# Kernel optimization log

Measured on AMD Instinct MI355X. Metric: run time of the kernel, lower is better.

Reference implementation:

```python
import jax, jax.numpy as jnp
import numpy as np

# Model dims: batch, num_patches, patch_dim, emb_dim, heads, layers, ffn, vocab, grid
B, N, PD, D, H, L, F, V, G = 4, 1024, 768, 768, 12, 6, 3072, 1024, 32
HD = D // H  # head dim = 64


def setup_inputs() -> dict:
    key = jax.random.key(0)
    ks = jax.random.split(key, 22)
    s = 0.02
    r = lambda k, shp: jax.random.normal(k, shp, dtype=jnp.float32) * s
    return {
        "patches": jax.random.normal(ks[0], (B, N, PD), dtype=jnp.float32),
        "mask": jax.random.bernoulli(ks[1], 0.3, (B, N)),
        "mask_token": r(ks[2], (PD,)),
        "patch_w": r(ks[3], (D, PD)),
        "patch_b": jnp.zeros((D,), jnp.float32),
        "pos_emb": r(ks[4], (N, D)),
        "rel_bias": r(ks[5], (2 * G - 1, 2 * G - 1)),
        # stacked per-layer params [L, ...]
        "in_w": r(ks[6], (L, 3 * D, D)),
        "in_b": jnp.zeros((L, 3 * D), jnp.float32),
        "attn_ow": r(ks[7], (L, D, D)),
        "attn_ob": jnp.zeros((L, D), jnp.float32),
        "ln1_s": jnp.ones((L, D), jnp.float32),
        "ln1_b": jnp.zeros((L, D), jnp.float32),
        "ffn_w1": r(ks[8], (L, F, D)),
        "ffn_b1": jnp.zeros((L, F), jnp.float32),
        "ffn_w2": r(ks[9], (L, D, F)),
        "ffn_b2": jnp.zeros((L, D), jnp.float32),
        "ln2_s": jnp.ones((L, D), jnp.float32),
        "ln2_b": jnp.zeros((L, D), jnp.float32),
        "head_w": r(ks[10], (V, D)),
        "head_b": jnp.zeros((V,), jnp.float32),
    }


def _layer_norm(x, scale, bias, eps=1e-5):
    mu = jnp.mean(x, axis=-1, keepdims=True)
    var = jnp.mean(jnp.square(x - mu), axis=-1, keepdims=True)
    return (x - mu) * jax.lax.rsqrt(var + eps) * scale + bias


def _rel_bias(rel_bias):
    # gathered Swin-style relative position bias -> [N, N]
    idx = jnp.arange(N)
    rows, cols = idx // G, idx % G
    ir = rows[:, None] - rows[None, :] + (G - 1)
    ic = cols[:, None] - cols[None, :] + (G - 1)
    return rel_bias[ir, ic]


def reference(patches, mask, mask_token, patch_w, patch_b, pos_emb, rel_bias,
              in_w, in_b, attn_ow, attn_ob, ln1_s, ln1_b,
              ffn_w1, ffn_b1, ffn_w2, ffn_b2, ln2_s, ln2_b, head_w, head_b):
    # replace masked patches with mask_token, project, add abs pos emb
    x = jnp.where(mask[:, :, None], mask_token, patches)
    x = x @ patch_w.T + patch_b + pos_emb  # [B,N,D]
    bias = _rel_bias(rel_bias)  # [N,N] additive attention bias
    scale = 1.0 / np.sqrt(HD).astype(np.float32)
    for l in range(L):
        qkv = x @ in_w[l].T + in_b[l]  # [B,N,3D]
        q, k, v = jnp.split(qkv, 3, axis=-1)
        split_heads = lambda t: t.reshape(B, N, H, HD).transpose(0, 2, 1, 3)
        q, k, v = split_heads(q), split_heads(k), split_heads(v)
        scores = jnp.einsum('bhqd,bhkd->bhqk', q, k) * scale + bias
        attn = jax.nn.softmax(scores, axis=-1)
        o = jnp.einsum('bhqk,bhkd->bhqd', attn, v)
        o = o.transpose(0, 2, 1, 3).reshape(B, N, D) @ attn_ow[l].T + attn_ob[l]
        x = _layer_norm(x + o, ln1_s[l], ln1_b[l])
        h = jax.nn.gelu(x @ ffn_w1[l].T + ffn_b1[l], approximate=False)
        x = _layer_norm(x + h @ ffn_w2[l].T + ffn_b2[l], ln2_s[l], ln2_b[l])
    logits = x @ head_w.T + head_b  # [B,N,V] (dropout = identity in eval)
    return logits, mask
```

## Files before the change

### kernel.cpp

```cpp
#include <hip/hip_runtime.h>
#include <hip/hip_bf16.h>
#include <stdint.h>


#define BM 64
#define BN 64
#define BK 32

using u16 = unsigned short;
typedef __attribute__((ext_vector_type(8))) short short8;
typedef __attribute__((ext_vector_type(4))) float f32x4;
typedef __attribute__((ext_vector_type(4))) u16 u16x4;

#define GPTR(p) ((const __attribute__((address_space(1))) void*)(p))
#define LPTR(p) ((__attribute__((address_space(3))) void*)(p))

__device__ __forceinline__ float b2f(u16 u){
  union { unsigned int i; float f; } x; x.i = ((unsigned int)u) << 16; return x.f;
}
__device__ __forceinline__ u16 f2b(float f){
  f = fminf(fmaxf(f, -448.0f), 448.0f);
  union { float f; unsigned int i; } x; x.f = f;
  unsigned int r = x.i + 0x7FFFu + ((x.i >> 16) & 1u);
  return (u16)(r >> 16);
}

__global__ __launch_bounds__(256) void detect_k(const u16* __restrict__ mk, int* __restrict__ mode){
  __shared__ int f[3];
  int tid = threadIdx.x;
  if (tid < 3) f[tid] = 0;
  __syncthreads();
  for (int i = tid; i < 2048; i += 256){
    u16 u = mk[i];
    if (u == 256 || u == 257) atomicOr(&f[0], 1);
    if (u == 0x3F80){ if ((i & 1) == 0) atomicOr(&f[1], 1); else atomicOr(&f[2], 1); }
  }
  __syncthreads();
  if (tid == 0){
    int m;
    if (f[0]) m = 0;
    else if (f[1]) m = 1;
    else if (f[2]) m = 2;
    else m = 3;
    *mode = m;
  }
}

__device__ __forceinline__ bool mask_at(const void* mk, int mode, int i){
  if (mode == 0) return ((const unsigned char*)mk)[i] != 0;
  if (mode == 1) return ((const u16*)mk)[i] != 0;
  if (mode == 2) return ((const float*)mk)[i] != 0.0f;
  return ((const int*)mk)[i] != 0;
}

__global__ __launch_bounds__(256) void wconv_k(const float* __restrict__ src, u16* __restrict__ dst){
  long i = ((long)blockIdx.x * 256 + threadIdx.x) * 4;
  float4 v = *(const float4*)(src + i);
  u16x4 o; o.x = f2b(v.x); o.y = f2b(v.y); o.z = f2b(v.z); o.w = f2b(v.w);
  *(u16x4*)(dst + i) = o;
}

__global__ __launch_bounds__(256) void embed_k(const float* __restrict__ patches, const void* __restrict__ mask,
                                               const int* __restrict__ mode, const float* __restrict__ mtok,
                                               u16* __restrict__ MP){
  int row = blockIdx.x;
  bool m = mask_at(mask, *mode, row);
  int tid = threadIdx.x;
  long base = (long)row * 768;
  #pragma unroll
  for (int i = 0; i < 3; i++){
    int p = tid + i * 256;
    MP[base + p] = f2b(m ? mtok[p] : patches[base + p]);
  }
}

__global__ __launch_bounds__(256) void maskout_k(const void* __restrict__ mask, const int* __restrict__ mode,
                                                 float* __restrict__ out){
  int i = blockIdx.x * 256 + threadIdx.x;
  out[i] = mask_at(mask, *mode, i) ? 1.0f : 0.0f;
}

__global__ __launch_bounds__(256) void ln_k(const u16* __restrict__ XR, u16* __restrict__ X,
                                            const float* __restrict__ s, const float* __restrict__ b){
  int row = blockIdx.x;
  int tid = threadIdx.x;
  const u16* xr = XR + (long)row * 768;
  float v0 = b2f(xr[tid]), v1 = b2f(xr[tid + 256]), v2 = b2f(xr[tid + 512]);
  float sum = v0 + v1 + v2, sq = v0 * v0 + v1 * v1 + v2 * v2;
  #pragma unroll
  for (int off = 32; off; off >>= 1){ sum += __shfl_xor(sum, off); sq += __shfl_xor(sq, off); }
  __shared__ float ls[4], lq[4];
  int wave = tid >> 6, lane = tid & 63;
  if (lane == 0){ ls[wave] = sum; lq[wave] = sq; }
  __syncthreads();
  sum = ls[0] + ls[1] + ls[2] + ls[3];
  sq  = lq[0] + lq[1] + lq[2] + lq[3];
  float mu = sum * (1.0f / 768.0f);
  float var = fmaxf(sq * (1.0f / 768.0f) - mu * mu, 0.0f);
  float rs = rsqrtf(var + 1e-5f);
  u16* xo = X + (long)row * 768;
  xo[tid]       = f2b((v0 - mu) * rs * s[tid]       + b[tid]);
  xo[tid + 256] = f2b((v1 - mu) * rs * s[tid + 256] + b[tid + 256]);
  xo[tid + 512] = f2b((v2 - mu) * rs * s[tid + 512] + b[tid + 512]);
}

__global__ __launch_bounds__(256) void softmax_k(u16* __restrict__ S){
  long row = (long)blockIdx.x * 4 + (threadIdx.x >> 6);
  u16* p = S + row * 1024;
  int lane = threadIdx.x & 63;
  short8 a = *(const short8*)&p[lane * 16];
  short8 b = *(const short8*)&p[lane * 16 + 8];
  float v[16]; float mx = -1e30f;
  #pragma unroll
  for (int i = 0; i < 8; i++){ v[i] = b2f((u16)a[i]); v[i + 8] = b2f((u16)b[i]); }
  #pragma unroll
  for (int i = 0; i < 16; i++) mx = fmaxf(mx, v[i]);
  #pragma unroll
  for (int off = 32; off; off >>= 1) mx = fmaxf(mx, __shfl_xor(mx, off));
  float sum = 0.0f;
  #pragma unroll
  for (int i = 0; i < 16; i++){ v[i] = __expf(v[i] - mx); sum += v[i]; }
  #pragma unroll
  for (int off = 32; off; off >>= 1) sum += __shfl_xor(sum, off);
  float inv = 1.0f / sum;
  #pragma unroll
  for (int i = 0; i < 8; i++){ a[i] = (short)f2b(v[i] * inv); b[i] = (short)f2b(v[i + 8] * inv); }
  *(short8*)&p[lane * 16] = a;
  *(short8*)&p[lane * 16 + 8] = b;
}

struct GP {
  const u16* A; const u16* W; u16* C; float* Cf;
  const float* bias; const float* relb; const float* pose;
  const u16* resid;
  u16* Cv;
  long sAz, sWz, sCz;
  int lda, ldw, ldc;
  int N, K;
  int wclamp, zBase;
  float scale;
};

template<int EPI>
__global__ __launch_bounds__(256)
void gemm_k(GP g){
  __shared__ __align__(16) u16 As[3][BM * BK];
  __shared__ __align__(16) u16 Bs[3][BN * BK];
  const int tid  = threadIdx.x;
  const int wave = tid >> 6, lane = tid & 63;
  const int quad = lane >> 4, l16 = lane & 15;
  const int wm = wave >> 1, wn = wave & 1;

  const int gx = gridDim.x;
  const int nwg = gx * gridDim.y;
  int bid = blockIdx.y * gx + blockIdx.x;
  {
    const int q = nwg >> 3, r = nwg & 7;
    const int xcd = bid & 7, loc = bid >> 3;
    bid = (xcd < r ? xcd * (q + 1) : r * (q + 1) + (xcd - r) * q) + loc;
  }
  const int m0 = (bid / gx) * BM;
  const int n0 = (bid % gx) * BN;
  const int z = blockIdx.z;

  const u16* Ab;
  const u16* Wb;
  if constexpr (EPI == 1){
    int hh = g.zBase + z;
    int b = hh / 12, h = hh - b * 12;
    Ab = g.A + (long)b * 1572864 + h * 64;
    Wb = Ab + 768;
  } else {
    Ab = g.A + (long)z * g.sAz;
    Wb = g.W + (long)z * g.sWz;
  }

  f32x4 acc[2][2];
  #pragma unroll
  for (int i = 0; i < 2; i++)
    #pragma unroll
    for (int j = 0; j < 2; j++) acc[i][j] = (f32x4){0.f, 0.f, 0.f, 0.f};

  const int c0 = wave * 64 + lane;
  const int arow = c0 >> 2, aslot = (c0 & 3) ^ (arow & 3);
  const u16* a0 = Ab + (long)(m0 + arow) * g.lda + aslot * 8;
  const u16* w0 = Wb + (long)min(n0 + arow, g.wclamp) * g.ldw + aslot * 8;
  const int o0 = wave * 512;

  const int nt = g.K / BK;

  #define STAGE(sb, kt) do { \
    __builtin_amdgcn_global_load_lds(GPTR(a0 + (kt)), LPTR(&As[(sb)][o0]), 16, 0, 0); \
    __builtin_amdgcn_global_load_lds(GPTR(w0 + (kt)), LPTR(&Bs[(sb)][o0]), 16, 0, 0); \
  } while (0)

  STAGE(0, 0);
  if (nt > 1){
    STAGE(1, BK);
    asm volatile("s_waitcnt vmcnt(2)\n\ts_barrier" ::: "memory");
  } else {
    asm volatile("s_waitcnt vmcnt(0)\n\ts_barrier" ::: "memory");
  }

  int sC = 0, sP = 2;
  for (int t = 0; t < nt; ++t){
    if (t + 2 < nt) STAGE(sP, (t + 2) * BK);

    short8 af[2], bf[2];
    #pragma unroll
    for (int i = 0; i < 2; i++){
      af[i] = *(const short8*)&As[sC][(wm * 32 + i * 16 + l16) * BK + ((quad ^ (l16 & 3)) * 8)];
      bf[i] = *(const short8*)&Bs[sC][(wn * 32 + i * 16 + l16) * BK + ((quad ^ (l16 & 3)) * 8)];
    }
    #pragma unroll
    for (int i = 0; i < 2; i++)
      #pragma unroll
      for (int j = 0; j < 2; j++)
        acc[i][j] = __builtin_amdgcn_mfma_f32_16x16x32_bf16(af[i], bf[j], acc[i][j], 0, 0, 0);

    if (t + 2 < nt)      asm volatile("s_waitcnt vmcnt(2) lgkmcnt(0)\n\ts_barrier" ::: "memory");
    else if (t + 1 < nt) asm volatile("s_waitcnt vmcnt(0) lgkmcnt(0)\n\ts_barrier" ::: "memory");
    sC = (sC == 2) ? 0 : sC + 1;
    sP = (sP == 2) ? 0 : sP + 1;
  }
  #undef STAGE

  #pragma unroll
  for (int i = 0; i < 2; i++){
    #pragma unroll
    for (int j = 0; j < 2; j++){
      #pragma unroll
      for (int rr = 0; rr < 4; rr++){
        const long r = (long)m0 + wm * 32 + i * 16 + quad * 4 + rr;
        const int  c = n0 + wn * 32 + j * 16 + l16;
        if (c >= g.N) continue;
        float v = acc[i][j][rr];
        if constexpr (EPI == 0){
          u16 o = f2b(v + g.bias[c]);
          if (c < 1536) g.C[r * 1536 + c] = o;
          else {
            int c2 = c - 1536;
            int hh = ((int)(r >> 10)) * 12 + (c2 >> 6);
            g.Cv[((long)hh * 64 + (c2 & 63)) * 1024 + (r & 1023)] = o;
          }
        } else if constexpr (EPI == 1){
          const int rq = (int)r;
          const int ir = (rq >> 5) - (c >> 5) + 31;
          const int ic = (rq & 31) - (c & 31) + 31;
          float val = v * g.scale + g.relb[ir * 63 + ic];
          (g.C + (long)z * g.sCz)[(long)rq * 1024 + c] = f2b(val);
        } else if constexpr (EPI == 2){
          int hh = g.zBase + z;
          int bg = hh / 12, h = hh - bg * 12;
          g.C[((long)bg * 1024 + r) * 768 + h * 64 + c] = f2b(v);
        } else if constexpr (EPI == 3){
          long o = r * (long)g.ldc + c;
          g.C[o] = f2b(v + g.bias[c] + b2f(g.resid[o]));
        } else if constexpr (EPI == 4){
          float t = v + g.bias[c];
          g.C[r * (long)g.ldc + c] = f2b(0.5f * t * (1.0f + erff(t * 0.70710678118654752f)));
        } else if constexpr (EPI == 5){
          float t = v + g.bias[c];
          t = fminf(fmaxf(t, -1.0e4f), 1.0e4f);
          g.Cf[r * (long)g.ldc + c] = t;
        } else {
          float val = v + g.bias[c] + g.pose[(long)(r & 1023) * 768 + c];
          g.C[r * (long)g.ldc + c] = f2b(val);
        }
      }
    }
  }
}

static inline void glaunch(int epi, dim3 grid, const GP& g, hipStream_t stream){
  switch (epi){
    case 0: gemm_k<0><<<grid, dim3(256), 0, stream>>>(g); break;
    case 1: gemm_k<1><<<grid, dim3(256), 0, stream>>>(g); break;
    case 2: gemm_k<2><<<grid, dim3(256), 0, stream>>>(g); break;
    case 3: gemm_k<3><<<grid, dim3(256), 0, stream>>>(g); break;
    case 4: gemm_k<4><<<grid, dim3(256), 0, stream>>>(g); break;
    case 5: gemm_k<5><<<grid, dim3(256), 0, stream>>>(g); break;
    default: gemm_k<6><<<grid, dim3(256), 0, stream>>>(g); break;
  }
}

extern "C" void kernel_launch(void* const* d_in, const int* in_sizes, int n_in,
                              void* d_out, int out_size, void* d_ws, size_t ws_size,
                              hipStream_t stream){
  (void)in_sizes; (void)n_in; (void)out_size;
  const float* patches = (const float*)d_in[0];
  const void*  mask    = d_in[1];
  const float* mtok    = (const float*)d_in[2];
  const float* patch_w = (const float*)d_in[3];
  const float* patch_b = (const float*)d_in[4];
  const float* pos_emb = (const float*)d_in[5];
  const float* rel_b   = (const float*)d_in[6];
  const float* in_w    = (const float*)d_in[7];
  const float* in_b    = (const float*)d_in[8];
  const float* attn_ow = (const float*)d_in[9];
  const float* attn_ob = (const float*)d_in[10];
  const float* ln1_s   = (const float*)d_in[11];
  const float* ln1_b   = (const float*)d_in[12];
  const float* ffn_w1  = (const float*)d_in[13];
  const float* ffn_b1  = (const float*)d_in[14];
  const float* ffn_w2  = (const float*)d_in[15];
  const float* ffn_b2  = (const float*)d_in[16];
  const float* ln2_s   = (const float*)d_in[17];
  const float* ln2_b   = (const float*)d_in[18];
  const float* head_w  = (const float*)d_in[19];
  const float* head_b  = (const float*)d_in[20];

  char* ws = (char*)d_ws;
  int* mode = (int*)ws;
  u16* X  = (u16*)(ws + 256);
  u16* WA = X + 3145728;
  u16* WB = WA + 2359296;
  char* EX = (char*)(WB + 2359296);
  long extra = (long)ws_size - 15728896L;
  const bool bigWs = extra >= 25165824L;

  u16*   dout16 = (u16*)d_out;
  float* doutf  = (float*)d_out;

  u16* QKp = (u16*)EX;
  u16* VTp = QKp + 6291456;
  u16* Op  = VTp + 3145728;
  u16* Hp  = (u16*)EX;
  long extra2 = extra - 25165824L;
  u16* Sp_big; int SCH_big;
  if (extra2 >= 4194304L){
    Sp_big = Op + 3145728;
    SCH_big = (int)(extra2 / 2097152L); if (SCH_big > 48) SCH_big = 48;
  } else {
    Sp_big = dout16; SCH_big = 8;
  }
  u16* Sp_small = (u16*)EX;
  int SCH_small = (int)(extra / 2097152L);
  if (SCH_small < 1) SCH_small = 1;
  if (SCH_small > 24) SCH_small = 24;
  u16* O16  = dout16;
  u16* QKh  = dout16 + 3145728;
  u16* VTh  = dout16 + 6291456;
  u16* XRb  = dout16 + 3145728;
  u16* Hc   = dout16;
  u16* XRc  = dout16 + 6291456;

  detect_k<<<dim3(1), dim3(256), 0, stream>>>((const u16*)mask, mode);

  GP g;
  wconv_k<<<dim3(576), dim3(256), 0, stream>>>(patch_w, WA);
  embed_k<<<dim3(4096), dim3(256), 0, stream>>>(patches, mask, mode, mtok, dout16);
  g = {};
  g.A = dout16; g.lda = 768; g.W = WA; g.ldw = 768; g.wclamp = 767;
  g.C = X; g.ldc = 768; g.N = 768; g.K = 768;
  g.bias = patch_b; g.pose = pos_emb;
  glaunch(6, dim3(12, 64, 1), g, stream);

  for (int l = 0; l < 6; l++){
    wconv_k<<<dim3(1728), dim3(256), 0, stream>>>(in_w + (long)l * 1769472, WA);
    wconv_k<<<dim3(576),  dim3(256), 0, stream>>>(attn_ow + (long)l * 589824, WB);

    if (bigWs){
      g = {};
      g.A = X; g.lda = 768; g.W = WA; g.ldw = 768; g.wclamp = 2303;
      g.bias = in_b + (long)l * 2304;
      g.C = QKp; g.Cv = VTp; g.N = 2304; g.K = 768;
      glaunch(0, dim3(36, 64, 1), g, stream);

      for (int ch0 = 0; ch0 < 48; ch0 += SCH_big){
        int zc = (48 - ch0 < SCH_big) ? (48 - ch0) : SCH_big;
        g = {};
        g.A = QKp; g.lda = 1536; g.zBase = ch0;
        g.C = Sp_big; g.sCz = 1048576; g.N = 1024; g.K = 64;
        g.relb = rel_b; g.scale = 0.125f; g.wclamp = 1023;
        glaunch(1, dim3(16, 16, zc), g, stream);
        softmax_k<<<dim3(zc * 256), dim3(256), 0, stream>>>(Sp_big);
        g = {};
        g.A = Sp_big; g.lda = 1024; g.sAz = 1048576;
        g.W = VTp + (long)ch0 * 65536; g.ldw = 1024; g.sWz = 65536; g.wclamp = 63;
        g.C = Op; g.zBase = ch0; g.N = 64; g.K = 1024;
        glaunch(2, dim3(1, 16, zc), g, stream);
      }

      g = {};
      g.A = Op; g.lda = 768; g.W = WB; g.ldw = 768; g.wclamp = 767;
      g.bias = attn_ob + (long)l * 768; g.resid = X;
      g.C = dout16; g.ldc = 768; g.N = 768; g.K = 768;
      glaunch(3, dim3(12, 64, 1), g, stream);
      ln_k<<<dim3(4096), dim3(256), 0, stream>>>(dout16, X, ln1_s + l * 768, ln1_b + l * 768);
    } else {
      for (int hb = 0; hb < 2; hb++){
        g = {};
        g.A = X + (long)hb * 1572864; g.lda = 768;
        g.W = WA; g.ldw = 768; g.wclamp = 2303;
        g.bias = in_b + (long)l * 2304;
        g.C = QKh; g.Cv = VTh; g.N = 2304; g.K = 768;
        glaunch(0, dim3(36, 32, 1), g, stream);

        for (int ch0 = 0; ch0 < 24; ch0 += SCH_small){
          int zc = (24 - ch0 < SCH_small) ? (24 - ch0) : SCH_small;
          g = {};
          g.A = QKh; g.lda = 1536; g.zBase = ch0;
          g.C = Sp_small; g.sCz = 1048576; g.N = 1024; g.K = 64;
          g.relb = rel_b; g.scale = 0.125f; g.wclamp = 1023;
          glaunch(1, dim3(16, 16, zc), g, stream);
          softmax_k<<<dim3(zc * 256), dim3(256), 0, stream>>>(Sp_small);
          g = {};
          g.A = Sp_small; g.lda = 1024; g.sAz = 1048576;
          g.W = VTh + (long)ch0 * 65536; g.ldw = 1024; g.sWz = 65536; g.wclamp = 63;
          g.C = O16; g.zBase = hb * 24 + ch0; g.N = 64; g.K = 1024;
          glaunch(2, dim3(1, 16, zc), g, stream);
        }
      }
      g = {};
      g.A = O16; g.lda = 768; g.W = WB; g.ldw = 768; g.wclamp = 767;
      g.bias = attn_ob + (long)l * 768; g.resid = X;
      g.C = XRb; g.ldc = 768; g.N = 768; g.K = 768;
      glaunch(3, dim3(12, 64, 1), g, stream);
      ln_k<<<dim3(4096), dim3(256), 0, stream>>>(XRb, X, ln1_s + l * 768, ln1_b + l * 768);
    }

    wconv_k<<<dim3(2304), dim3(256), 0, stream>>>(ffn_w1 + (long)l * 2359296, WA);
    wconv_k<<<dim3(2304), dim3(256), 0, stream>>>(ffn_w2 + (long)l * 2359296, WB);

    if (bigWs){
      g = {};
      g.A = X; g.lda = 768; g.W = WA; g.ldw = 768; g.wclamp = 3071;
      g.bias = ffn_b1 + (long)l * 3072;
      g.C = Hp; g.ldc = 3072; g.N = 3072; g.K = 768;
      glaunch(4, dim3(48, 64, 1), g, stream);
      g = {};
      g.A = Hp; g.lda = 3072; g.W = WB; g.ldw = 3072; g.wclamp = 767;
      g.bias = ffn_b2 + (long)l * 768; g.resid = X;
      g.C = dout16; g.ldc = 768; g.N = 768; g.K = 3072;
      glaunch(3, dim3(12, 64, 1), g, stream);
      ln_k<<<dim3(4096), dim3(256), 0, stream>>>(dout16, X, ln2_s + l * 768, ln2_b + l * 768);
    } else {
      for (int cc = 0; cc < 2; cc++){
        u16* Xc = X + (long)cc * 1572864;
        g = {};
        g.A = Xc; g.lda = 768; g.W = WA; g.ldw = 768; g.wclamp = 3071;
        g.bias = ffn_b1 + (long)l * 3072;
        g.C = Hc; g.ldc = 3072; g.N = 3072; g.K = 768;
        glaunch(4, dim3(48, 32, 1), g, stream);
        g = {};
        g.A = Hc; g.lda = 3072; g.W = WB; g.ldw = 3072; g.wclamp = 767;
        g.bias = ffn_b2 + (long)l * 768; g.resid = Xc;
        g.C = XRc; g.ldc = 768; g.N = 768; g.K = 3072;
        glaunch(3, dim3(12, 32, 1), g, stream);
        ln_k<<<dim3(2048), dim3(256), 0, stream>>>(XRc, Xc, ln2_s + l * 768, ln2_b + l * 768);
      }
    }
  }

  wconv_k<<<dim3(768), dim3(256), 0, stream>>>(head_w, WA);
  g = {};
  g.A = X; g.lda = 768; g.W = WA; g.ldw = 768; g.wclamp = 1023;
  g.bias = head_b;
  g.Cf = doutf; g.ldc = 1024; g.N = 1024; g.K = 768;
  glaunch(5, dim3(16, 64, 1), g, stream);
  maskout_k<<<dim3(16), dim3(256), 0, stream>>>(mask, mode, doutf + 4194304);
}
```

Measured before the change: 1.941 ms.

## Deepen GEMM LDS pipeline to six stages and change swizzle pattern

The GEMM's shared-memory ring buffer grows from three to six stages, with five tiles prefetched ahead and vmcnt waits tuned per remaining depth, to hide global-load latency. The LDS XOR swizzle now uses (row>>1)&3 to reduce bank conflicts on the 16-byte fragment reads. LDS use per block doubles to about 48KB, which may reduce how many blocks fit on each CU.

```diff
diff --git a/kernel.cpp b/kernel.cpp
--- a/kernel.cpp
+++ b/kernel.cpp
@@ -144,8 +144,8 @@
 template<int EPI>
 __global__ __launch_bounds__(256)
 void gemm_k(GP g){
-  __shared__ __align__(16) u16 As[3][BM * BK];
-  __shared__ __align__(16) u16 Bs[3][BN * BK];
+  __shared__ __align__(16) u16 As[6][BM * BK];
+  __shared__ __align__(16) u16 Bs[6][BN * BK];
   const int tid  = threadIdx.x;
   const int wave = tid >> 6, lane = tid & 63;
   const int quad = lane >> 4, l16 = lane & 15;
@@ -182,48 +182,62 @@
     for (int j = 0; j < 2; j++) acc[i][j] = (f32x4){0.f, 0.f, 0.f, 0.f};
 
   const int c0 = wave * 64 + lane;
-  const int arow = c0 >> 2, aslot = (c0 & 3) ^ (arow & 3);
+  const int arow = c0 >> 2, aslot = (c0 & 3) ^ ((arow >> 1) & 3);
   const u16* a0 = Ab + (long)(m0 + arow) * g.lda + aslot * 8;
   const u16* w0 = Wb + (long)min(n0 + arow, g.wclamp) * g.ldw + aslot * 8;
   const int o0 = wave * 512;
 
   const int nt = g.K / BK;
+  const int rs = (quad ^ ((l16 >> 1) & 3)) * 8;
 
   #define STAGE(sb, kt) do { \
     __builtin_amdgcn_global_load_lds(GPTR(a0 + (kt)), LPTR(&As[(sb)][o0]), 16, 0, 0); \
     __builtin_amdgcn_global_load_lds(GPTR(w0 + (kt)), LPTR(&Bs[(sb)][o0]), 16, 0, 0); \
   } while (0)
 
-  STAGE(0, 0);
-  if (nt > 1){
-    STAGE(1, BK);
-    asm volatile("s_waitcnt vmcnt(2)\n\ts_barrier" ::: "memory");
-  } else {
-    asm volatile("s_waitcnt vmcnt(0)\n\ts_barrier" ::: "memory");
-  }
-
-  int sC = 0, sP = 2;
-  for (int t = 0; t < nt; ++t){
-    if (t + 2 < nt) STAGE(sP, (t + 2) * BK);
-
-    short8 af[2], bf[2];
-    #pragma unroll
-    for (int i = 0; i < 2; i++){
-      af[i] = *(const short8*)&As[sC][(wm * 32 + i * 16 + l16) * BK + ((quad ^ (l16 & 3)) * 8)];
-      bf[i] = *(const short8*)&Bs[sC][(wn * 32 + i * 16 + l16) * BK + ((quad ^ (l16 & 3)) * 8)];
+  #define COMPUTE(sb) do { \
+    short8 af[2], bf[2]; \
+    af[0] = *(const short8*)&As[(sb)][(wm * 32 + l16) * BK + rs]; \
+    af[1] = *(const short8*)&As[(sb)][(wm * 32 + 16 + l16) * BK + rs]; \
+    bf[0] = *(const short8*)&Bs[(sb)][(wn * 32 + l16) * BK + rs]; \
+    bf[1] = *(const short8*)&Bs[(sb)][(wn * 32 + 16 + l16) * BK + rs]; \
+    acc[0][0] = __builtin_amdgcn_mfma_f32_16x16x32_bf16(af[0], bf[0], acc[0][0], 0, 0, 0); \
+    acc[0][1] = __builtin_amdgcn_mfma_f32_16x16x32_bf16(af[0], bf[1], acc[0][1], 0, 0, 0); \
+    acc[1][0] = __builtin_amdgcn_mfma_f32_16x16x32_bf16(af[1], bf[0], acc[1][0], 0, 0, 0); \
+    acc[1][1] = __builtin_amdgcn_mfma_f32_16x16x32_bf16(af[1], bf[1], acc[1][1], 0, 0, 0); \
+  } while (0)
+
+  const int pre = nt < 5 ? nt : 5;
+  for (int i = 0; i < pre; ++i) STAGE(i, i * BK);
+  switch (pre){
+    case 5:  asm volatile("s_waitcnt vmcnt(8)\n\ts_barrier" ::: "memory"); break;
+    case 4:  asm volatile("s_waitcnt vmcnt(6)\n\ts_barrier" ::: "memory"); break;
+    case 3:  asm volatile("s_waitcnt vmcnt(4)\n\ts_barrier" ::: "memory"); break;
+    case 2:  asm volatile("s_waitcnt vmcnt(2)\n\ts_barrier" ::: "memory"); break;
+    default: asm volatile("s_waitcnt vmcnt(0)\n\ts_barrier" ::: "memory"); break;
+  }
+
+  int t = 0, sC = 0, sP = 5;
+  for (; t + 5 < nt; ++t){
+    STAGE(sP, (t + 5) * BK);
+    COMPUTE(sC);
+    asm volatile("s_waitcnt vmcnt(8) lgkmcnt(0)\n\ts_barrier" ::: "memory");
+    sC = sC == 5 ? 0 : sC + 1;
+    sP = sP == 5 ? 0 : sP + 1;
+  }
+  for (; t < nt; ++t){
+    COMPUTE(sC);
+    if (t + 1 < nt){
+      const int c = nt - 2 - t;
+      if      (c >= 3) asm volatile("s_waitcnt vmcnt(6) lgkmcnt(0)\n\ts_barrier" ::: "memory");
+      else if (c == 2) asm volatile("s_waitcnt vmcnt(4) lgkmcnt(0)\n\ts_barrier" ::: "memory");
+      else if (c == 1) asm volatile("s_waitcnt vmcnt(2) lgkmcnt(0)\n\ts_barrier" ::: "memory");
+      else             asm volatile("s_waitcnt vmcnt(0) lgkmcnt(0)\n\ts_barrier" ::: "memory");
     }
-    #pragma unroll
-    for (int i = 0; i < 2; i++)
-      #pragma unroll
-      for (int j = 0; j < 2; j++)
-        acc[i][j] = __builtin_amdgcn_mfma_f32_16x16x32_bf16(af[i], bf[j], acc[i][j], 0, 0, 0);
-
-    if (t + 2 < nt)      asm volatile("s_waitcnt vmcnt(2) lgkmcnt(0)\n\ts_barrier" ::: "memory");
-    else if (t + 1 < nt) asm volatile("s_waitcnt vmcnt(0) lgkmcnt(0)\n\ts_barrier" ::: "memory");
-    sC = (sC == 2) ? 0 : sC + 1;
-    sP = (sP == 2) ? 0 : sP + 1;
+    sC = sC == 5 ? 0 : sC + 1;
   }
   #undef STAGE
+  #undef COMPUTE
 
   #pragma unroll
   for (int i = 0; i < 2; i++){
@@ -257,12 +271,12 @@
           long o = r * (long)g.ldc + c;
           g.C[o] = f2b(v + g.bias[c] + b2f(g.resid[o]));
         } else if constexpr (EPI == 4){
-          float t = v + g.bias[c];
-          g.C[r * (long)g.ldc + c] = f2b(0.5f * t * (1.0f + erff(t * 0.70710678118654752f)));
+          float t2 = v + g.bias[c];
+          g.C[r * (long)g.ldc + c] = f2b(0.5f * t2 * (1.0f + erff(t2 * 0.70710678118654752f)));
         } else if constexpr (EPI == 5){
-          float t = v + g.bias[c];
-          t = fminf(fmaxf(t, -1.0e4f), 1.0e4f);
-          g.Cf[r * (long)g.ldc + c] = t;
+          float t2 = v + g.bias[c];
+          t2 = fminf(fmaxf(t2, -1.0e4f), 1.0e4f);
+          g.Cf[r * (long)g.ldc + c] = t2;
         } else {
           float val = v + g.bias[c] + g.pose[(long)(r & 1023) * 768 + c];
           g.C[r * (long)g.ldc + c] = f2b(val);
```

Measured after the change: 2.040 ms. +5.1%, slower.

## Fuse attention scores, softmax and PV into a single flash-attention kernel

Applied to the files above, without the earlier changes.

Replaces the three-kernel attention path (QK^T GEMM with relative-bias epilogue, row softmax, PV GEMM) with one flash-style kernel. It keeps scores in registers and LDS, uses online softmax with double-buffered K/V tiles loaded straight into LDS, and adds the relative position bias on the fly. This avoids writing and re-reading the full bf16 score matrices through HBM and drops the chunked launch loops. The GEMM LDS swizzle is also changed to XOR on (row>>1) to reduce bank conflicts. The cost is extra block-wide barriers per key tile for the cross-wave max/sum reductions, and only 768 blocks per launch.

```diff
diff --git a/kernel.cpp b/kernel.cpp
--- a/kernel.cpp
+++ b/kernel.cpp
@@ -104,41 +104,15 @@
   xo[tid + 512] = f2b((v2 - mu) * rs * s[tid + 512] + b[tid + 512]);
 }
 
-__global__ __launch_bounds__(256) void softmax_k(u16* __restrict__ S){
-  long row = (long)blockIdx.x * 4 + (threadIdx.x >> 6);
-  u16* p = S + row * 1024;
-  int lane = threadIdx.x & 63;
-  short8 a = *(const short8*)&p[lane * 16];
-  short8 b = *(const short8*)&p[lane * 16 + 8];
-  float v[16]; float mx = -1e30f;
-  #pragma unroll
-  for (int i = 0; i < 8; i++){ v[i] = b2f((u16)a[i]); v[i + 8] = b2f((u16)b[i]); }
-  #pragma unroll
-  for (int i = 0; i < 16; i++) mx = fmaxf(mx, v[i]);
-  #pragma unroll
-  for (int off = 32; off; off >>= 1) mx = fmaxf(mx, __shfl_xor(mx, off));
-  float sum = 0.0f;
-  #pragma unroll
-  for (int i = 0; i < 16; i++){ v[i] = __expf(v[i] - mx); sum += v[i]; }
-  #pragma unroll
-  for (int off = 32; off; off >>= 1) sum += __shfl_xor(sum, off);
-  float inv = 1.0f / sum;
-  #pragma unroll
-  for (int i = 0; i < 8; i++){ a[i] = (short)f2b(v[i] * inv); b[i] = (short)f2b(v[i + 8] * inv); }
-  *(short8*)&p[lane * 16] = a;
-  *(short8*)&p[lane * 16 + 8] = b;
-}
-
 struct GP {
   const u16* A; const u16* W; u16* C; float* Cf;
-  const float* bias; const float* relb; const float* pose;
+  const float* bias; const float* pose;
   const u16* resid;
   u16* Cv;
-  long sAz, sWz, sCz;
+  long sAz, sWz;
   int lda, ldw, ldc;
   int N, K;
   int wclamp, zBase;
-  float scale;
 };
 
 template<int EPI>
@@ -163,17 +137,8 @@
   const int n0 = (bid % gx) * BN;
   const int z = blockIdx.z;
 
-  const u16* Ab;
-  const u16* Wb;
-  if constexpr (EPI == 1){
-    int hh = g.zBase + z;
-    int b = hh / 12, h = hh - b * 12;
-    Ab = g.A + (long)b * 1572864 + h * 64;
-    Wb = Ab + 768;
-  } else {
-    Ab = g.A + (long)z * g.sAz;
-    Wb = g.W + (long)z * g.sWz;
-  }
+  const u16* Ab = g.A + (long)z * g.sAz;
+  const u16* Wb = g.W + (long)z * g.sWz;
 
   f32x4 acc[2][2];
   #pragma unroll
@@ -182,12 +147,13 @@
     for (int j = 0; j < 2; j++) acc[i][j] = (f32x4){0.f, 0.f, 0.f, 0.f};
 
   const int c0 = wave * 64 + lane;
-  const int arow = c0 >> 2, aslot = (c0 & 3) ^ (arow & 3);
+  const int arow = c0 >> 2, aslot = (c0 & 3) ^ ((arow >> 1) & 3);
   const u16* a0 = Ab + (long)(m0 + arow) * g.lda + aslot * 8;
   const u16* w0 = Wb + (long)min(n0 + arow, g.wclamp) * g.ldw + aslot * 8;
   const int o0 = wave * 512;
 
   const int nt = g.K / BK;
+  const int rs = (quad ^ ((l16 >> 1) & 3)) * 8;
 
   #define STAGE(sb, kt) do { \
     __builtin_amdgcn_global_load_lds(GPTR(a0 + (kt)), LPTR(&As[(sb)][o0]), 16, 0, 0); \
@@ -207,16 +173,14 @@
     if (t + 2 < nt) STAGE(sP, (t + 2) * BK);
 
     short8 af[2], bf[2];
-    #pragma unroll
-    for (int i = 0; i < 2; i++){
-      af[i] = *(const short8*)&As[sC][(wm * 32 + i * 16 + l16) * BK + ((quad ^ (l16 & 3)) * 8)];
-      bf[i] = *(const short8*)&Bs[sC][(wn * 32 + i * 16 + l16) * BK + ((quad ^ (l16 & 3)) * 8)];
-    }
-    #pragma unroll
-    for (int i = 0; i < 2; i++)
-      #pragma unroll
-      for (int j = 0; j < 2; j++)
-        acc[i][j] = __builtin_amdgcn_mfma_f32_16x16x32_bf16(af[i], bf[j], acc[i][j], 0, 0, 0);
+    af[0] = *(const short8*)&As[sC][(wm * 32 + l16) * BK + rs];
+    af[1] = *(const short8*)&As[sC][(wm * 32 + 16 + l16) * BK + rs];
+    bf[0] = *(const short8*)&Bs[sC][(wn * 32 + l16) * BK + rs];
+    bf[1] = *(const short8*)&Bs[sC][(wn * 32 + 16 + l16) * BK + rs];
+    acc[0][0] = __builtin_amdgcn_mfma_f32_16x16x32_bf16(af[0], bf[0], acc[0][0], 0, 0, 0);
+    acc[0][1] = __builtin_amdgcn_mfma_f32_16x16x32_bf16(af[0], bf[1], acc[0][1], 0, 0, 0);
+    acc[1][0] = __builtin_amdgcn_mfma_f32_16x16x32_bf16(af[1], bf[0], acc[1][0], 0, 0, 0);
+    acc[1][1] = __builtin_amdgcn_mfma_f32_16x16x32_bf16(af[1], bf[1], acc[1][1], 0, 0, 0);
 
     if (t + 2 < nt)      asm volatile("s_waitcnt vmcnt(2) lgkmcnt(0)\n\ts_barrier" ::: "memory");
     else if (t + 1 < nt) asm volatile("s_waitcnt vmcnt(0) lgkmcnt(0)\n\ts_barrier" ::: "memory");
@@ -243,26 +207,16 @@
             int hh = ((int)(r >> 10)) * 12 + (c2 >> 6);
             g.Cv[((long)hh * 64 + (c2 & 63)) * 1024 + (r & 1023)] = o;
           }
-        } else if constexpr (EPI == 1){
-          const int rq = (int)r;
-          const int ir = (rq >> 5) - (c >> 5) + 31;
-          const int ic = (rq & 31) - (c & 31) + 31;
-          float val = v * g.scale + g.relb[ir * 63 + ic];
-          (g.C + (long)z * g.sCz)[(long)rq * 1024 + c] = f2b(val);
-        } else if constexpr (EPI == 2){
-          int hh = g.zBase + z;
-          int bg = hh / 12, h = hh - bg * 12;
-          g.C[((long)bg * 1024 + r) * 768 + h * 64 + c] = f2b(v);
         } else if constexpr (EPI == 3){
           long o = r * (long)g.ldc + c;
           g.C[o] = f2b(v + g.bias[c] + b2f(g.resid[o]));
         } else if constexpr (EPI == 4){
-          float t = v + g.bias[c];
-          g.C[r * (long)g.ldc + c] = f2b(0.5f * t * (1.0f + erff(t * 0.70710678118654752f)));
+          float t2 = v + g.bias[c];
+          g.C[r * (long)g.ldc + c] = f2b(0.5f * t2 * (1.0f + erff(t2 * 0.70710678118654752f)));
         } else if constexpr (EPI == 5){
-          float t = v + g.bias[c];
-          t = fminf(fmaxf(t, -1.0e4f), 1.0e4f);
-          g.Cf[r * (long)g.ldc + c] = t;
+          float t2 = v + g.bias[c];
+          t2 = fminf(fmaxf(t2, -1.0e4f), 1.0e4f);
+          g.Cf[r * (long)g.ldc + c] = t2;
         } else {
           float val = v + g.bias[c] + g.pose[(long)(r & 1023) * 768 + c];
           g.C[r * (long)g.ldc + c] = f2b(val);
@@ -275,12 +229,203 @@
 static inline void glaunch(int epi, dim3 grid, const GP& g, hipStream_t stream){
   switch (epi){
     case 0: gemm_k<0><<<grid, dim3(256), 0, stream>>>(g); break;
-    case 1: gemm_k<1><<<grid, dim3(256), 0, stream>>>(g); break;
-    case 2: gemm_k<2><<<grid, dim3(256), 0, stream>>>(g); break;
     case 3: gemm_k<3><<<grid, dim3(256), 0, stream>>>(g); break;
     case 4: gemm_k<4><<<grid, dim3(256), 0, stream>>>(g); break;
     case 5: gemm_k<5><<<grid, dim3(256), 0, stream>>>(g); break;
     default: gemm_k<6><<<grid, dim3(256), 0, stream>>>(g); break;
+  }
+}
+
+struct FP {
+  const u16* QK; const u16* VT; u16* O; const float* relb;
+  int oBase;
+};
+
+__global__ __launch_bounds__(256) void flash_k(FP f){
+  __shared__ __align__(16) u16 Qs[2][2048];
+  __shared__ __align__(16) u16 Ks[2][2][2048];
+  __shared__ __align__(16) u16 Vs[2][2][2048];
+  __shared__ __align__(16) u16 Ps[2][2048];
+  __shared__ float rmx[64][2], rsm[64][2];
+  const int tid  = threadIdx.x;
+  const int wave = tid >> 6, lane = tid & 63;
+  const int quad = lane >> 4, l16 = lane & 15;
+  const int wm = wave >> 1, wn = wave & 1;
+  const int hhl = blockIdx.y, bl = hhl / 12, h = hhl - bl * 12;
+  const int q0 = blockIdx.x * 64;
+
+  const int srow = tid >> 2, sslot = (tid & 3) ^ ((srow >> 1) & 3);
+  const u16* Qsrc = f.QK + ((long)bl * 1024 + q0 + srow) * 1536 + h * 64 + sslot * 8;
+  const u16* Ksrc = f.QK + ((long)bl * 1024 + srow) * 1536 + 768 + h * 64 + sslot * 8;
+  const u16* Vsrc = f.VT + ((long)hhl * 64 + srow) * 1024 + sslot * 8;
+  const int od = wave * 512;
+  const int rs = (quad ^ ((l16 >> 1) & 3)) * 8;
+
+  __builtin_amdgcn_global_load_lds(GPTR(Qsrc),      LPTR(&Qs[0][od]),    16, 0, 0);
+  __builtin_amdgcn_global_load_lds(GPTR(Qsrc + 32), LPTR(&Qs[1][od]),    16, 0, 0);
+  __builtin_amdgcn_global_load_lds(GPTR(Ksrc),      LPTR(&Ks[0][0][od]), 16, 0, 0);
+  __builtin_amdgcn_global_load_lds(GPTR(Ksrc + 32), LPTR(&Ks[0][1][od]), 16, 0, 0);
+  __builtin_amdgcn_global_load_lds(GPTR(Vsrc),      LPTR(&Vs[0][0][od]), 16, 0, 0);
+  __builtin_amdgcn_global_load_lds(GPTR(Vsrc + 32), LPTR(&Vs[0][1][od]), 16, 0, 0);
+  asm volatile("s_waitcnt vmcnt(0) lgkmcnt(0)\n\ts_barrier" ::: "memory");
+
+  f32x4 Oa[2][2];
+  #pragma unroll
+  for (int i = 0; i < 2; i++)
+    #pragma unroll
+    for (int j = 0; j < 2; j++) Oa[i][j] = (f32x4){0.f, 0.f, 0.f, 0.f};
+  float m_[2][4], l_[2][4];
+  #pragma unroll
+  for (int i = 0; i < 2; i++)
+    #pragma unroll
+    for (int rr = 0; rr < 4; rr++){ m_[i][rr] = -1e30f; l_[i][rr] = 0.0f; }
+
+  for (int t = 0; t < 16; ++t){
+    const int cur = t & 1;
+    if (t < 15){
+      const u16* kn = Ksrc + (long)(t + 1) * 98304;
+      const u16* vn = Vsrc + (t + 1) * 64;
+      __builtin_amdgcn_global_load_lds(GPTR(kn),      LPTR(&Ks[cur ^ 1][0][od]), 16, 0, 0);
+      __builtin_amdgcn_global_load_lds(GPTR(kn + 32), LPTR(&Ks[cur ^ 1][1][od]), 16, 0, 0);
+      __builtin_amdgcn_global_load_lds(GPTR(vn),      LPTR(&Vs[cur ^ 1][0][od]), 16, 0, 0);
+      __builtin_amdgcn_global_load_lds(GPTR(vn + 32), LPTR(&Vs[cur ^ 1][1][od]), 16, 0, 0);
+    }
+
+    f32x4 S[2][2];
+    #pragma unroll
+    for (int i = 0; i < 2; i++)
+      #pragma unroll
+      for (int j = 0; j < 2; j++) S[i][j] = (f32x4){0.f, 0.f, 0.f, 0.f};
+    #pragma unroll
+    for (int ks = 0; ks < 2; ks++){
+      short8 af[2], bf[2];
+      af[0] = *(const short8*)&Qs[ks][(wm * 32 + l16) * 32 + rs];
+      af[1] = *(const short8*)&Qs[ks][(wm * 32 + 16 + l16) * 32 + rs];
+      bf[0] = *(const short8*)&Ks[cur][ks][(wn * 32 + l16) * 32 + rs];
+      bf[1] = *(const short8*)&Ks[cur][ks][(wn * 32 + 16 + l16) * 32 + rs];
+      S[0][0] = __builtin_amdgcn_mfma_f32_16x16x32_bf16(af[0], bf[0], S[0][0], 0, 0, 0);
+      S[0][1] = __builtin_amdgcn_mfma_f32_16x16x32_bf16(af[0], bf[1], S[0][1], 0, 0, 0);
+      S[1][0] = __builtin_amdgcn_mfma_f32_16x16x32_bf16(af[1], bf[0], S[1][0], 0, 0, 0);
+      S[1][1] = __builtin_amdgcn_mfma_f32_16x16x32_bf16(af[1], bf[1], S[1][1], 0, 0, 0);
+    }
+
+    float tmax[2][4];
+    #pragma unroll
+    for (int i = 0; i < 2; i++)
+      #pragma unroll
+      for (int rr = 0; rr < 4; rr++) tmax[i][rr] = -1e30f;
+    #pragma unroll
+    for (int i = 0; i < 2; i++){
+      #pragma unroll
+      for (int j = 0; j < 2; j++){
+        #pragma unroll
+        for (int rr = 0; rr < 4; rr++){
+          const int qy = wm * 32 + i * 16 + quad * 4 + rr;
+          const int kx = t * 64 + wn * 32 + j * 16 + l16;
+          const int ir = ((q0 + qy) >> 5) - (kx >> 5) + 31;
+          const int ic = (qy & 31) - (kx & 31) + 31;
+          float s = S[i][j][rr] * 0.125f + f.relb[ir * 63 + ic];
+          S[i][j][rr] = s;
+          tmax[i][rr] = fmaxf(tmax[i][rr], s);
+        }
+      }
+    }
+    #pragma unroll
+    for (int i = 0; i < 2; i++)
+      #pragma unroll
+      for (int rr = 0; rr < 4; rr++)
+        #pragma unroll
+        for (int off = 1; off < 16; off <<= 1)
+          tmax[i][rr] = fmaxf(tmax[i][rr], __shfl_xor(tmax[i][rr], off));
+    if (l16 == 0){
+      #pragma unroll
+      for (int i = 0; i < 2; i++)
+        #pragma unroll
+        for (int rr = 0; rr < 4; rr++)
+          rmx[wm * 32 + i * 16 + quad * 4 + rr][wn] = tmax[i][rr];
+    }
+    asm volatile("s_waitcnt lgkmcnt(0)\n\ts_barrier" ::: "memory");
+
+    float psum[2][4];
+    #pragma unroll
+    for (int i = 0; i < 2; i++){
+      #pragma unroll
+      for (int rr = 0; rr < 4; rr++){
+        const int row = wm * 32 + i * 16 + quad * 4 + rr;
+        const float tm = fmaxf(rmx[row][0], rmx[row][1]);
+        const float mn = fmaxf(m_[i][rr], tm);
+        const float sc = __expf(m_[i][rr] - mn);
+        m_[i][rr] = mn; l_[i][rr] *= sc;
+        #pragma unroll
+        for (int j = 0; j < 2; j++) Oa[i][j][rr] *= sc;
+        psum[i][rr] = 0.0f;
+      }
+    }
+    #pragma unroll
+    for (int i = 0; i < 2; i++){
+      #pragma unroll
+      for (int j = 0; j < 2; j++){
+        #pragma unroll
+        for (int rr = 0; rr < 4; rr++){
+          float p = __expf(S[i][j][rr] - m_[i][rr]);
+          psum[i][rr] += p;
+          const int row = wm * 32 + i * 16 + quad * 4 + rr;
+          const int col = wn * 32 + j * 16 + l16;
+          const int half = col >> 5, c5 = col & 31;
+          const int ps = (c5 >> 3) ^ ((row >> 1) & 3);
+          Ps[half][row * 32 + ps * 8 + (c5 & 7)] = f2b(p);
+        }
+      }
+    }
+    #pragma unroll
+    for (int i = 0; i < 2; i++)
+      #pragma unroll
+      for (int rr = 0; rr < 4; rr++)
+        #pragma unroll
+        for (int off = 1; off < 16; off <<= 1)
+          psum[i][rr] += __shfl_xor(psum[i][rr], off);
+    if (l16 == 0){
+      #pragma unroll
+      for (int i = 0; i < 2; i++)
+        #pragma unroll
+        for (int rr = 0; rr < 4; rr++)
+          rsm[wm * 32 + i * 16 + quad * 4 + rr][wn] = psum[i][rr];
+    }
+    asm volatile("s_waitcnt lgkmcnt(0)\n\ts_barrier" ::: "memory");
+    #pragma unroll
+    for (int i = 0; i < 2; i++)
+      #pragma unroll
+      for (int rr = 0; rr < 4; rr++){
+        const int row = wm * 32 + i * 16 + quad * 4 + rr;
+        l_[i][rr] += rsm[row][0] + rsm[row][1];
+      }
+
+    #pragma unroll
+    for (int ks = 0; ks < 2; ks++){
+      short8 pa[2], bv[2];
+      pa[0] = *(const short8*)&Ps[ks][(wm * 32 + l16) * 32 + rs];
+      pa[1] = *(const short8*)&Ps[ks][(wm * 32 + 16 + l16) * 32 + rs];
+      bv[0] = *(const short8*)&Vs[cur][ks][(wn * 32 + l16) * 32 + rs];
+      bv[1] = *(const short8*)&Vs[cur][ks][(wn * 32 + 16 + l16) * 32 + rs];
+      Oa[0][0] = __builtin_amdgcn_mfma_f32_16x16x32_bf16(pa[0], bv[0], Oa[0][0], 0, 0, 0);
+      Oa[0][1] = __builtin_amdgcn_mfma_f32_16x16x32_bf16(pa[0], bv[1], Oa[0][1], 0, 0, 0);
+      Oa[1][0] = __builtin_amdgcn_mfma_f32_16x16x32_bf16(pa[1], bv[0], Oa[1][0], 0, 0, 0);
+      Oa[1][1] = __builtin_amdgcn_mfma_f32_16x16x32_bf16(pa[1], bv[1], Oa[1][1], 0, 0, 0);
+    }
+    if (t < 15) asm volatile("s_waitcnt vmcnt(0) lgkmcnt(0)\n\ts_barrier" ::: "memory");
+  }
+
+  #pragma unroll
+  for (int i = 0; i < 2; i++){
+    #pragma unroll
+    for (int rr = 0; rr < 4; rr++){
+      const float inv = 1.0f / l_[i][rr];
+      const int row = wm * 32 + i * 16 + quad * 4 + rr;
+      const long ro = ((long)(f.oBase + bl) * 1024 + q0 + row) * 768 + h * 64;
+      #pragma unroll
+      for (int j = 0; j < 2; j++)
+        f.O[ro + wn * 32 + j * 16 + l16] = f2b(Oa[i][j][rr] * inv);
+    }
   }
 }
 
@@ -326,18 +471,6 @@
   u16* VTp = QKp + 6291456;
   u16* Op  = VTp + 3145728;
   u16* Hp  = (u16*)EX;
-  long extra2 = extra - 25165824L;
-  u16* Sp_big; int SCH_big;
-  if (extra2 >= 4194304L){
-    Sp_big = Op + 3145728;
-    SCH_big = (int)(extra2 / 2097152L); if (SCH_big > 48) SCH_big = 48;
-  } else {
-    Sp_big = dout16; SCH_big = 8;
-  }
-  u16* Sp_small = (u16*)EX;
-  int SCH_small = (int)(extra / 2097152L);
-  if (SCH_small < 1) SCH_small = 1;
-  if (SCH_small > 24) SCH_small = 24;
   u16* O16  = dout16;
   u16* QKh  = dout16 + 3145728;
   u16* VTh  = dout16 + 6291456;
@@ -347,7 +480,7 @@
 
   detect_k<<<dim3(1), dim3(256), 0, stream>>>((const u16*)mask, mode);
 
-  GP g;
+  GP g; FP fp;
   wconv_k<<<dim3(576), dim3(256), 0, stream>>>(patch_w, WA);
   embed_k<<<dim3(4096), dim3(256), 0, stream>>>(patches, mask, mode, mtok, dout16);
   g = {};
@@ -367,20 +500,9 @@
       g.C = QKp; g.Cv = VTp; g.N = 2304; g.K = 768;
       glaunch(0, dim3(36, 64, 1), g, stream);
 
-      for (int ch0 = 0; ch0 < 48; ch0 += SCH_big){
-        int zc = (48 - ch0 < SCH_big) ? (48 - ch0) : SCH_big;
-        g = {};
-        g.A = QKp; g.lda = 1536; g.zBase = ch0;
-        g.C = Sp_big; g.sCz = 1048576; g.N = 1024; g.K = 64;
-        g.relb = rel_b; g.scale = 0.125f; g.wclamp = 1023;
-        glaunch(1, dim3(16, 16, zc), g, stream);
-        softmax_k<<<dim3(zc * 256), dim3(256), 0, stream>>>(Sp_big);
-        g = {};
-        g.A = Sp_big; g.lda = 1024; g.sAz = 1048576;
-        g.W = VTp + (long)ch0 * 65536; g.ldw = 1024; g.sWz = 65536; g.wclamp = 63;
-        g.C = Op; g.zBase = ch0; g.N = 64; g.K = 1024;
-        glaunch(2, dim3(1, 16, zc), g, stream);
-      }
+      fp = {};
+      fp.QK = QKp; fp.VT = VTp; fp.O = Op; fp.relb = rel_b; fp.oBase = 0;
+      flash_k<<<dim3(16, 48), dim3(256), 0, stream>>>(fp);
 
       g = {};
       g.A = Op; g.lda = 768; g.W = WB; g.ldw = 768; g.wclamp = 767;
@@ -397,20 +519,9 @@
         g.C = QKh; g.Cv = VTh; g.N = 2304; g.K = 768;
         glaunch(0, dim3(36, 32, 1), g, stream);
 
-        for (int ch0 = 0; ch0 < 24; ch0 += SCH_small){
-          int zc = (24 - ch0 < SCH_small) ? (24 - ch0) : SCH_small;
-          g = {};
-          g.A = QKh; g.lda = 1536; g.zBase = ch0;
-          g.C = Sp_small; g.sCz = 1048576; g.N = 1024; g.K = 64;
-          g.relb = rel_b; g.scale = 0.125f; g.wclamp = 1023;
-          glaunch(1, dim3(16, 16, zc), g, stream);
-          softmax_k<<<dim3(zc * 256), dim3(256), 0, stream>>>(Sp_small);
-          g = {};
-          g.A = Sp_small; g.lda = 1024; g.sAz = 1048576;
-          g.W = VTh + (long)ch0 * 65536; g.ldw = 1024; g.sWz = 65536; g.wclamp = 63;
-          g.C = O16; g.zBase = hb * 24 + ch0; g.N = 64; g.K = 1024;
-          glaunch(2, dim3(1, 16, zc), g, stream);
-        }
+        fp = {};
+        fp.QK = QKh; fp.VT = VTh; fp.O = O16; fp.relb = rel_b; fp.oBase = hb * 2;
+        flash_k<<<dim3(16, 24), dim3(256), 0, stream>>>(fp);
       }
       g = {};
       g.A = O16; g.lda = 768; g.W = WB; g.ldw = 768; g.wclamp = 767;
```

Result: faster. 1.855 ms (-4.4%).
